# Performance work log

Measured on AMD Instinct MI355X. Metric: run time of the kernel, lower is better.

Reference implementation:

```python
import jax, jax.numpy as jnp
import numpy as np

NUM_USERS = 50000
NUM_ITEMS = 20000
NUM_NODES = NUM_USERS + NUM_ITEMS
FEAT_DIM = 768
HID = 128
NUM_LAYERS = 3
N_EDGES = 2_000_000
LN_EPS = 1e-5


def setup_inputs() -> dict:
    key = jax.random.key(0)
    ks = jax.random.split(key, 12)
    edge_index = jax.random.randint(ks[0], (2, N_EDGES), 0, NUM_NODES, dtype=jnp.int64) if jax.config.jax_enable_x64 else jax.random.randint(ks[0], (2, N_EDGES), 0, NUM_NODES, dtype=jnp.int32)
    item_features = jax.random.normal(ks[1], (NUM_ITEMS, FEAT_DIM), dtype=jnp.float32)
    embedding = jax.random.normal(ks[2], (NUM_NODES, HID), dtype=jnp.float32) * 0.1
    W1 = jax.random.normal(ks[3], (FEAT_DIM, 512), dtype=jnp.float32) * 0.02
    b1 = jnp.zeros((512,), jnp.float32)
    g1 = jnp.ones((512,), jnp.float32)
    be1 = jnp.zeros((512,), jnp.float32)
    W2 = jax.random.normal(ks[4], (512, HID), dtype=jnp.float32) * 0.02
    b2 = jnp.zeros((HID,), jnp.float32)
    g2 = jnp.ones((HID,), jnp.float32)
    be2 = jnp.zeros((HID,), jnp.float32)
    W3 = jax.random.normal(ks[5], (HID, HID), dtype=jnp.float32) * 0.02
    b3 = jnp.zeros((HID,), jnp.float32)
    meta_weight = jnp.asarray(0.01, jnp.float32)
    return {"edge_index": edge_index, "item_features": item_features, "embedding": embedding,
            "W1": W1, "b1": b1, "g1": g1, "be1": be1,
            "W2": W2, "b2": b2, "g2": g2, "be2": be2,
            "W3": W3, "b3": b3, "meta_weight": meta_weight}


def _layer_norm(x, g, b):
    mu = jnp.mean(x, axis=-1, keepdims=True)
    var = jnp.mean(jnp.square(x - mu), axis=-1, keepdims=True)
    return (x - mu) * jax.lax.rsqrt(var + LN_EPS) * g + b


def reference(edge_index, item_features, embedding, W1, b1, g1, be1, W2, b2, g2, be2, W3, b3, meta_weight):
    # item metadata MLP (eval mode: dropout is identity)
    h = jax.nn.relu(_layer_norm(item_features @ W1 + b1, g1, be1))
    h = jax.nn.relu(_layer_norm(h @ W2 + b2, g2, be2))
    h = h @ W3 + b3
    # F.normalize(p=2, dim=-1)
    item_meta = h / jnp.maximum(jnp.linalg.norm(h, axis=-1, keepdims=True), 1e-12)

    # fuse metadata into item id embeddings
    e0 = jnp.concatenate([embedding[:NUM_USERS],
                          embedding[NUM_USERS:] + meta_weight * item_meta], axis=0)

    src, dst = edge_index[0], edge_index[1]
    # symmetric GCN normalization: deg from destination counts
    deg = jax.ops.segment_sum(jnp.ones(src.shape[0], e0.dtype), dst, num_segments=NUM_NODES)
    dinv = jnp.where(deg > 0, jax.lax.rsqrt(jnp.maximum(deg, 1.0)), 0.0)
    norm = (dinv[src] * dinv[dst])[:, None]  # [E, 1]

    alpha = 1.0 / (NUM_LAYERS + 1)
    out = e0 * alpha
    x = e0
    for _ in range(NUM_LAYERS):
        x = jax.ops.segment_sum(x[src] * norm, dst, num_segments=NUM_NODES)
        out = out + x * alpha
    return out
```

## Files before the change

### kernel.cpp

```cpp
#include <hip/hip_runtime.h>
#include <hip/hip_bf16.h>

#define NUM_USERS 50000
#define NUM_ITEMS 20000
#define NUM_NODES (NUM_USERS + NUM_ITEMS)
#define FEAT_DIM 768
#define HID 128
#define H1DIM 512
#define LN_EPS 1e-5f
#define ALPHA 0.25f
#define NBKT 137

typedef __attribute__((ext_vector_type(8))) short short8;
typedef __attribute__((ext_vector_type(4))) float floatx4;

static __device__ inline unsigned short f2bf(float f) {
  unsigned int u = __float_as_uint(f);
  u += 0x7fffu + ((u >> 16) & 1u);
  return (unsigned short)(u >> 16);
}
static __device__ inline float bflo(unsigned int u) {
  return __uint_as_float(u << 16);
}
static __device__ inline float bfhi(unsigned int u) {
  return __uint_as_float(u & 0xffff0000u);
}

__global__ __launch_bounds__(256) void cast_bf16(
    const float* __restrict__ in, unsigned short* __restrict__ out) {
  size_t i = (size_t)blockIdx.x * 256 + threadIdx.x;
  float4 u = ((const float4*)in)[i * 2];
  float4 v = ((const float4*)in)[i * 2 + 1];
  union { unsigned short s[8]; uint4 q; } p;
  p.s[0] = f2bf(u.x); p.s[1] = f2bf(u.y); p.s[2] = f2bf(u.z); p.s[3] = f2bf(u.w);
  p.s[4] = f2bf(v.x); p.s[5] = f2bf(v.y); p.s[6] = f2bf(v.z); p.s[7] = f2bf(v.w);
  ((uint4*)out)[i] = p.q;
}

__global__ __launch_bounds__(256) void transpose_cast(
    const float* __restrict__ W, unsigned short* __restrict__ Wt,
    int K, int N) {
  __shared__ float tile[32][33];
  int tx = threadIdx.x, ty = threadIdx.y;
  int bx = blockIdx.x, by = blockIdx.y;
#pragma unroll
  for (int kk = 0; kk < 4; kk++)
    tile[ty + kk * 8][tx] = W[(size_t)(by * 32 + ty + kk * 8) * N + bx * 32 + tx];
  __syncthreads();
#pragma unroll
  for (int kk = 0; kk < 4; kk++)
    Wt[(size_t)(bx * 32 + ty + kk * 8) * K + by * 32 + tx] =
        f2bf(tile[tx][ty + kk * 8]);
}

__global__ __launch_bounds__(256) void gemm_mfma_bias(
    const unsigned short* __restrict__ A, const unsigned short* __restrict__ Bt,
    const float* __restrict__ bias, float* __restrict__ C,
    int M, int N, int K) {
  __shared__ __align__(16) unsigned short As[128 * 32];
  __shared__ __align__(16) unsigned short Bs[128 * 32];
  const int tid = threadIdx.x;
  const int wave = tid >> 6, lane = tid & 63;
  const int quad = lane >> 4, l16 = lane & 15;
  const int wm = wave >> 1, wn = wave & 1;
  const int bm = blockIdx.y * 128, bn = blockIdx.x * 128;

  floatx4 acc[4][4];
#pragma unroll
  for (int i = 0; i < 4; i++)
#pragma unroll
    for (int j = 0; j < 4; j++) acc[i][j] = (floatx4){0.f, 0.f, 0.f, 0.f};

  const int srow = lane >> 2;
  const int scol = (lane & 3) * 8;

  for (int k0 = 0; k0 < K; k0 += 32) {
#pragma unroll
    for (int i = 0; i < 2; i++) {
      int c = wave * 2 + i;
      int arow = bm + c * 16 + srow;
      if (arow >= M) arow = M - 1;
      const unsigned short* ga = A + (size_t)arow * K + k0 + scol;
      __builtin_amdgcn_global_load_lds(
          (const __attribute__((address_space(1))) unsigned int*)(uintptr_t)ga,
          (__attribute__((address_space(3))) unsigned int*)(uintptr_t)(As + c * 512),
          16, 0, 0);
      int brow = bn + c * 16 + srow;
      const unsigned short* gb = Bt + (size_t)brow * K + k0 + scol;
      __builtin_amdgcn_global_load_lds(
          (const __attribute__((address_space(1))) unsigned int*)(uintptr_t)gb,
          (__attribute__((address_space(3))) unsigned int*)(uintptr_t)(Bs + c * 512),
          16, 0, 0);
    }
    __syncthreads();

    short8 af[4], bf[4];
#pragma unroll
    for (int i = 0; i < 4; i++) {
      af[i] = *(const short8*)&As[(wm * 64 + i * 16 + l16) * 32 + quad * 8];
      bf[i] = *(const short8*)&Bs[(wn * 64 + i * 16 + l16) * 32 + quad * 8];
    }
#pragma unroll
    for (int i = 0; i < 4; i++)
#pragma unroll
      for (int j = 0; j < 4; j++)
        acc[i][j] = __builtin_amdgcn_mfma_f32_16x16x32_bf16(af[i], bf[j],
                                                            acc[i][j], 0, 0, 0);
    __syncthreads();
  }

#pragma unroll
  for (int i = 0; i < 4; i++) {
    int row0 = bm + wm * 64 + i * 16 + quad * 4;
#pragma unroll
    for (int j = 0; j < 4; j++) {
      int col = bn + wn * 64 + j * 16 + l16;
      float bv = bias[col];
#pragma unroll
      for (int r = 0; r < 4; r++) {
        int row = row0 + r;
        if (row < M) C[(size_t)row * N + col] = acc[i][j][r] + bv;
      }
    }
  }
}

__global__ __launch_bounds__(256) void ln_relu_w512_bf16(
    const float* __restrict__ X, const float* __restrict__ g,
    const float* __restrict__ be, unsigned short* __restrict__ O) {
  int row = blockIdx.x, t = threadIdx.x;
  const float* x = X + (size_t)row * H1DIM;
  float v0 = x[t], v1 = x[t + 256];
  float s = v0 + v1, q = v0 * v0 + v1 * v1;
#pragma unroll
  for (int off = 32; off > 0; off >>= 1) {
    s += __shfl_down(s, off);
    q += __shfl_down(q, off);
  }
  __shared__ float ss[4], qq[4];
  int lane = t & 63, wid = t >> 6;
  if (lane == 0) { ss[wid] = s; qq[wid] = q; }
  __syncthreads();
  float S = ss[0] + ss[1] + ss[2] + ss[3];
  float Q = qq[0] + qq[1] + qq[2] + qq[3];
  float mu = S * (1.f / 512.f);
  float var = Q * (1.f / 512.f) - mu * mu;
  float rs = rsqrtf(var + LN_EPS);
  float y0 = (v0 - mu) * rs * g[t] + be[t];
  float y1 = (v1 - mu) * rs * g[t + 256] + be[t + 256];
  unsigned short* o = O + (size_t)row * H1DIM;
  o[t] = f2bf(fmaxf(y0, 0.f));
  o[t + 256] = f2bf(fmaxf(y1, 0.f));
}

__global__ __launch_bounds__(256) void ln_relu_w128(
    float* __restrict__ X, const float* __restrict__ g,
    const float* __restrict__ be, int rows) {
  int gwid = (blockIdx.x * blockDim.x + threadIdx.x) >> 6;
  if (gwid >= rows) return;
  int lane = threadIdx.x & 63;
  float* x = X + (size_t)gwid * HID;
  float v0 = x[lane], v1 = x[lane + 64];
  float s = v0 + v1, q = v0 * v0 + v1 * v1;
#pragma unroll
  for (int off = 32; off > 0; off >>= 1) {
    s += __shfl_down(s, off);
    q += __shfl_down(q, off);
  }
  s = __shfl(s, 0);
  q = __shfl(q, 0);
  float mu = s * (1.f / 128.f);
  float var = q * (1.f / 128.f) - mu * mu;
  float rs = rsqrtf(var + LN_EPS);
  float y0 = (v0 - mu) * rs * g[lane] + be[lane];
  float y1 = (v1 - mu) * rs * g[lane + 64] + be[lane + 64];
  x[lane] = fmaxf(y0, 0.f);
  x[lane + 64] = fmaxf(y1, 0.f);
}

__global__ __launch_bounds__(128) void gemm3_norm4(
    const float* __restrict__ H, const float* __restrict__ W3,
    const float* __restrict__ b3, float* __restrict__ meta) {
  int r0 = blockIdx.x * 4, t = threadIdx.x;
  __shared__ float hrow[4][HID];
#pragma unroll
  for (int r = 0; r < 4; r++) hrow[r][t] = H[(size_t)(r0 + r) * HID + t];
  __syncthreads();
  float s0 = 0.f, s1 = 0.f, s2 = 0.f, s3 = 0.f;
#pragma unroll 4
  for (int k = 0; k < HID; k++) {
    float w = W3[k * HID + t];
    s0 = fmaf(hrow[0][k], w, s0);
    s1 = fmaf(hrow[1][k], w, s1);
    s2 = fmaf(hrow[2][k], w, s2);
    s3 = fmaf(hrow[3][k], w, s3);
  }
  float b = b3[t];
  s0 += b; s1 += b; s2 += b; s3 += b;
  float q0 = s0 * s0, q1 = s1 * s1, q2 = s2 * s2, q3 = s3 * s3;
#pragma unroll
  for (int off = 32; off > 0; off >>= 1) {
    q0 += __shfl_down(q0, off);
    q1 += __shfl_down(q1, off);
    q2 += __shfl_down(q2, off);
    q3 += __shfl_down(q3, off);
  }
  __shared__ float qs[4][2];
  if ((t & 63) == 0) {
    int w = t >> 6;
    qs[0][w] = q0; qs[1][w] = q1; qs[2][w] = q2; qs[3][w] = q3;
  }
  __syncthreads();
  float n0 = fmaxf(sqrtf(qs[0][0] + qs[0][1]), 1e-12f);
  float n1 = fmaxf(sqrtf(qs[1][0] + qs[1][1]), 1e-12f);
  float n2 = fmaxf(sqrtf(qs[2][0] + qs[2][1]), 1e-12f);
  float n3 = fmaxf(sqrtf(qs[3][0] + qs[3][1]), 1e-12f);
  meta[(size_t)(r0 + 0) * HID + t] = s0 / n0;
  meta[(size_t)(r0 + 1) * HID + t] = s1 / n1;
  meta[(size_t)(r0 + 2) * HID + t] = s2 / n2;
  meta[(size_t)(r0 + 3) * HID + t] = s3 / n3;
}

__global__ __launch_bounds__(256) void build_e0(
    const float* __restrict__ emb, const float* __restrict__ meta,
    const float* __restrict__ mw_p, float* __restrict__ x0,
    float* __restrict__ out) {
  size_t i = (size_t)blockIdx.x * 256 + threadIdx.x;
  float e = emb[i];
  size_t node = i >> 7;
  if (node >= NUM_USERS) e += mw_p[0] * meta[i - (size_t)NUM_USERS * HID];
  x0[i] = e;
  out[i] = ALPHA * e;
}

__global__ __launch_bounds__(256) void p1_hist(const int* __restrict__ dst,
                                               int* __restrict__ ghist,
                                               int E, int NBL) {
  __shared__ int h[NBKT];
  int t = threadIdx.x;
  if (t < NBKT) h[t] = 0;
  __syncthreads();
  int base = blockIdx.x * 8192;
  for (int i = t; i < 8192; i += 256) {
    int e = base + i;
    if (e < E) atomicAdd(&h[dst[e] >> 9], 1);
  }
  __syncthreads();
  if (t < NBKT) ghist[t * NBL + blockIdx.x] = h[t];
}

__global__ __launch_bounds__(256) void scan_a(const int* __restrict__ in,
                                              int* __restrict__ outp,
                                              int* __restrict__ bsum, int n) {
  int i = blockIdx.x * 256 + threadIdx.x;
  int v = (i < n) ? in[i] : 0;
  int lane = threadIdx.x & 63, wid = threadIdx.x >> 6;
  int s = v;
#pragma unroll
  for (int off = 1; off < 64; off <<= 1) {
    int u = __shfl_up(s, off);
    if (lane >= off) s += u;
  }
  __shared__ int wsum[4];
  if (lane == 63) wsum[wid] = s;
  __syncthreads();
  int add = 0;
  for (int w = 0; w < wid; w++) add += wsum[w];
  int incl = s + add;
  if (i < n) outp[i] = incl - v;
  if (threadIdx.x == 255) bsum[blockIdx.x] = incl;
}

__global__ __launch_bounds__(512) void scan_b(int* __restrict__ bsum, int nb) {
  int t = threadIdx.x;
  int v = (t < nb) ? bsum[t] : 0;
  int lane = t & 63, wid = t >> 6;
  int s = v;
#pragma unroll
  for (int off = 1; off < 64; off <<= 1) {
    int u = __shfl_up(s, off);
    if (lane >= off) s += u;
  }
  __shared__ int ws[8];
  if (lane == 63) ws[wid] = s;
  __syncthreads();
  int add = 0;
  for (int w = 0; w < wid; w++) add += ws[w];
  if (t < nb) bsum[t] = s + add - v;
}

__global__ __launch_bounds__(256) void scan_c(int* __restrict__ outp,
                                              const int* __restrict__ bsum,
                                              int n) {
  int i = blockIdx.x * 256 + threadIdx.x;
  if (i < n) outp[i] += bsum[blockIdx.x];
}

__global__ __launch_bounds__(256) void p1_scatter(
    const int* __restrict__ src, const int* __restrict__ dst,
    const int* __restrict__ gscan, unsigned long long* __restrict__ pairs,
    int E, int NBL) {
  __shared__ int cur[NBKT];
  int t = threadIdx.x;
  if (t < NBKT) cur[t] = gscan[t * NBL + blockIdx.x];
  __syncthreads();
  int base = blockIdx.x * 8192;
  for (int i = t; i < 8192; i += 256) {
    int e = base + i;
    if (e < E) {
      int d = dst[e];
      int pos = atomicAdd(&cur[d >> 9], 1);
      pairs[pos] = ((unsigned long long)(unsigned)d << 32) | (unsigned)src[e];
    }
  }
}

__global__ __launch_bounds__(512) void p2_build(
    const unsigned long long* __restrict__ pairs,
    const int* __restrict__ gscan, int* __restrict__ rowptr,
    int* __restrict__ csr_src, int E, int NBL) {
  __shared__ int hist[512];
  __shared__ int ws8[8];
  int b = blockIdx.x, t = threadIdx.x;
  int base = gscan[b * NBL];
  int end = (b == NBKT - 1) ? E : gscan[(b + 1) * NBL];
  hist[t] = 0;
  __syncthreads();
  for (int i = base + t; i < end; i += 512) {
    unsigned d = (unsigned)(pairs[i] >> 32);
    atomicAdd(&hist[d & 511], 1);
  }
  __syncthreads();
  int v = hist[t];
  int lane = t & 63, wid = t >> 6;
  int s = v;
#pragma unroll
  for (int off = 1; off < 64; off <<= 1) {
    int u = __shfl_up(s, off);
    if (lane >= off) s += u;
  }
  if (lane == 63) ws8[wid] = s;
  __syncthreads();
  int add = 0;
  for (int w = 0; w < wid; w++) add += ws8[w];
  int excl = s + add - v;
  int node = (b << 9) + t;
  if (node < NUM_NODES) rowptr[node] = base + excl;
  if (b == NBKT - 1 && t == 0) rowptr[NUM_NODES] = E;
  __syncthreads();
  hist[t] = base + excl;
  __syncthreads();
  for (int i = base + t; i < end; i += 512) {
    unsigned long long p = pairs[i];
    unsigned d = (unsigned)(p >> 32);
    int pos = atomicAdd(&hist[d & 511], 1);
    csr_src[pos] = (int)(unsigned)p;
  }
}

__global__ __launch_bounds__(256) void calc_dinv2(const int* __restrict__ rowptr,
                                                  float* __restrict__ dinv,
                                                  int n) {
  int i = blockIdx.x * 256 + threadIdx.x;
  if (i < n) {
    int d = rowptr[i + 1] - rowptr[i];
    dinv[i] = d > 0 ? rsqrtf((float)d) : 0.f;
  }
}

template <int XBF>
__global__ __launch_bounds__(256) void spmm_prop(
    const int* __restrict__ rowptr, const int* __restrict__ csr_src,
    const float* __restrict__ dinv, const void* __restrict__ xv,
    unsigned short* __restrict__ y, float* __restrict__ out, int write_y) {
  int wid = (blockIdx.x * 256 + threadIdx.x) >> 6;
  int lane = threadIdx.x & 63;
  int half = lane >> 5, q = lane & 31;
  int row = wid * 2 + half;
  int beg = rowptr[row], end = rowptr[row + 1];
  float wd = dinv[row];
  float a0 = 0.f, a1 = 0.f, a2 = 0.f, a3 = 0.f;
  int p = beg;
  if (XBF) {
    const unsigned short* xq = (const unsigned short*)xv + q * 4;
    for (; p + 4 <= end; p += 4) {
      int s0 = csr_src[p], s1 = csr_src[p + 1];
      int s2 = csr_src[p + 2], s3 = csr_src[p + 3];
      float c0 = dinv[s0], c1 = dinv[s1], c2 = dinv[s2], c3 = dinv[s3];
      uint2 v0 = *(const uint2*)(xq + (size_t)s0 * HID);
      uint2 v1 = *(const uint2*)(xq + (size_t)s1 * HID);
      uint2 v2 = *(const uint2*)(xq + (size_t)s2 * HID);
      uint2 v3 = *(const uint2*)(xq + (size_t)s3 * HID);
      a0 += c0 * bflo(v0.x) + c1 * bflo(v1.x) + c2 * bflo(v2.x) + c3 * bflo(v3.x);
      a1 += c0 * bfhi(v0.x) + c1 * bfhi(v1.x) + c2 * bfhi(v2.x) + c3 * bfhi(v3.x);
      a2 += c0 * bflo(v0.y) + c1 * bflo(v1.y) + c2 * bflo(v2.y) + c3 * bflo(v3.y);
      a3 += c0 * bfhi(v0.y) + c1 * bfhi(v1.y) + c2 * bfhi(v2.y) + c3 * bfhi(v3.y);
    }
    for (; p < end; p++) {
      int s0 = csr_src[p];
      float c0 = dinv[s0];
      uint2 v0 = *(const uint2*)(xq + (size_t)s0 * HID);
      a0 += c0 * bflo(v0.x); a1 += c0 * bfhi(v0.x);
      a2 += c0 * bflo(v0.y); a3 += c0 * bfhi(v0.y);
    }
  } else {
    const float* xq = (const float*)xv + q * 4;
    for (; p + 4 <= end; p += 4) {
      int s0 = csr_src[p], s1 = csr_src[p + 1];
      int s2 = csr_src[p + 2], s3 = csr_src[p + 3];
      float c0 = dinv[s0], c1 = dinv[s1], c2 = dinv[s2], c3 = dinv[s3];
      float4 v0 = *(const float4*)(xq + (size_t)s0 * HID);
      float4 v1 = *(const float4*)(xq + (size_t)s1 * HID);
      float4 v2 = *(const float4*)(xq + (size_t)s2 * HID);
      float4 v3 = *(const float4*)(xq + (size_t)s3 * HID);
      a0 += c0 * v0.x + c1 * v1.x + c2 * v2.x + c3 * v3.x;
      a1 += c0 * v0.y + c1 * v1.y + c2 * v2.y + c3 * v3.y;
      a2 += c0 * v0.z + c1 * v1.z + c2 * v2.z + c3 * v3.z;
      a3 += c0 * v0.w + c1 * v1.w + c2 * v2.w + c3 * v3.w;
    }
    for (; p < end; p++) {
      int s0 = csr_src[p];
      float c0 = dinv[s0];
      float4 v0 = *(const float4*)(xq + (size_t)s0 * HID);
      a0 += c0 * v0.x; a1 += c0 * v0.y; a2 += c0 * v0.z; a3 += c0 * v0.w;
    }
  }
  a0 *= wd; a1 *= wd; a2 *= wd; a3 *= wd;
  size_t o = (size_t)row * HID + q * 4;
  if (write_y) {
    union { unsigned short s[4]; uint2 u; } pk;
    pk.s[0] = f2bf(a0); pk.s[1] = f2bf(a1);
    pk.s[2] = f2bf(a2); pk.s[3] = f2bf(a3);
    *(uint2*)&y[o] = pk.u;
  }
  float4 po = *(const float4*)&out[o];
  po.x += ALPHA * a0; po.y += ALPHA * a1;
  po.z += ALPHA * a2; po.w += ALPHA * a3;
  *(float4*)&out[o] = po;
}

extern "C" void kernel_launch(void* const* d_in, const int* in_sizes, int n_in,
                              void* d_out, int out_size, void* d_ws,
                              size_t ws_size, hipStream_t stream) {
  const int* edge = (const int*)d_in[0];
  const float* item_feat = (const float*)d_in[1];
  const float* emb = (const float*)d_in[2];
  const float* W1 = (const float*)d_in[3];
  const float* b1 = (const float*)d_in[4];
  const float* g1 = (const float*)d_in[5];
  const float* be1 = (const float*)d_in[6];
  const float* W2 = (const float*)d_in[7];
  const float* b2 = (const float*)d_in[8];
  const float* g2 = (const float*)d_in[9];
  const float* be2 = (const float*)d_in[10];
  const float* W3 = (const float*)d_in[11];
  const float* b3 = (const float*)d_in[12];
  const float* mw = (const float*)d_in[13];
  float* out = (float*)d_out;

  const int E = in_sizes[0] / 2;
  const int* src = edge;
  const int* dst = edge + E;
  const int NBL = (E + 8191) / 8192;
  const int nScan = NBKT * NBL;
  const int NBs = (nScan + 255) / 256;

  char* ws = (char*)d_ws;
  float* h1 = (float*)(ws + 0);
  float* h2 = (float*)(ws + 40960000);
  unsigned short* h1b = (unsigned short*)(ws + 51200000);
  float* xAf = (float*)(ws + 51200000);
  unsigned short* Af = (unsigned short*)(ws + 87040000);
  unsigned short* xBb = (unsigned short*)(ws + 87040000);
  unsigned short* xCb = (unsigned short*)(ws + 104960000);
  unsigned short* W1t = (unsigned short*)(ws + 122880000);
  unsigned short* W2t = (unsigned short*)(ws + 123666432);
  float* meta = h1;

  unsigned long long* pairs = (unsigned long long*)(ws + 0);
  int* rowptr = (int*)(ws + 16000000);
  float* dinv = (float*)(ws + 16500000);
  int* ghist = (int*)(ws + 16800000);
  int* gscan = (int*)(ws + 17000000);
  int* bsum = (int*)(ws + 17200000);
  int* csr_src = (int*)(ws + 17500000);

  cast_bf16<<<(NUM_ITEMS * FEAT_DIM / 8) / 256, 256, 0, stream>>>(item_feat, Af);
  transpose_cast<<<dim3(H1DIM / 32, FEAT_DIM / 32), dim3(32, 8), 0, stream>>>(
      W1, W1t, FEAT_DIM, H1DIM);
  transpose_cast<<<dim3(HID / 32, H1DIM / 32), dim3(32, 8), 0, stream>>>(
      W2, W2t, H1DIM, HID);

  gemm_mfma_bias<<<dim3(H1DIM / 128, (NUM_ITEMS + 127) / 128), 256, 0, stream>>>(
      Af, W1t, b1, h1, NUM_ITEMS, H1DIM, FEAT_DIM);
  ln_relu_w512_bf16<<<NUM_ITEMS, 256, 0, stream>>>(h1, g1, be1, h1b);
  gemm_mfma_bias<<<dim3(HID / 128, (NUM_ITEMS + 127) / 128), 256, 0, stream>>>(
      h1b, W2t, b2, h2, NUM_ITEMS, HID, H1DIM);
  ln_relu_w128<<<(NUM_ITEMS * 64) / 256, 256, 0, stream>>>(h2, g2, be2,
                                                           NUM_ITEMS);
  gemm3_norm4<<<NUM_ITEMS / 4, 128, 0, stream>>>(h2, W3, b3, meta);

  build_e0<<<(NUM_NODES * HID) / 256, 256, 0, stream>>>(emb, meta, mw, xAf, out);

  p1_hist<<<NBL, 256, 0, stream>>>(dst, ghist, E, NBL);
  scan_a<<<NBs, 256, 0, stream>>>(ghist, gscan, bsum, nScan);
  scan_b<<<1, 512, 0, stream>>>(bsum, NBs);
  scan_c<<<NBs, 256, 0, stream>>>(gscan, bsum, nScan);
  p1_scatter<<<NBL, 256, 0, stream>>>(src, dst, gscan, pairs, E, NBL);
  p2_build<<<NBKT, 512, 0, stream>>>(pairs, gscan, rowptr, csr_src, E, NBL);
  calc_dinv2<<<(NUM_NODES + 255) / 256, 256, 0, stream>>>(rowptr, dinv,
                                                          NUM_NODES);

  const int PG = (NUM_NODES / 2 * 64) / 256;
  spmm_prop<0><<<PG, 256, 0, stream>>>(rowptr, csr_src, dinv, xAf, xBb, out, 1);
  spmm_prop<1><<<PG, 256, 0, stream>>>(rowptr, csr_src, dinv, xBb, xCb, out, 1);
  spmm_prop<1><<<PG, 256, 0, stream>>>(rowptr, csr_src, dinv, xCb, nullptr, out,
                                       0);
}
```

Baseline: 651.1 us.

## Store propagation features in chunk-major bf16 layout and split SpMM by feature chunk

The layer-0 features are now written as bf16 in a chunk-major layout (8 chunks of 16 features per node), and the SpMM kernel handles one feature chunk per block, with 8 lanes per row. Each chunk's gather footprint (about 2.2 MB) can then stay cache-resident while random source rows are read, instead of scattering across the full 128-wide rows. The cost is that each row's CSR indices and dinv values are re-read 8 times, one per chunk, and each gather is now 32 bytes. The first layer also reads bf16 instead of fp32, which lowers precision.

```diff
diff --git a/kernel.cpp b/kernel.cpp
--- a/kernel.cpp
+++ b/kernel.cpp
@@ -221,16 +221,25 @@
   meta[(size_t)(r0 + 3) * HID + t] = s3 / n3;
 }
 
-__global__ __launch_bounds__(256) void build_e0(
+__global__ __launch_bounds__(256) void build_e0_cm(
     const float* __restrict__ emb, const float* __restrict__ meta,
-    const float* __restrict__ mw_p, float* __restrict__ x0,
+    const float* __restrict__ mw_p, unsigned int* __restrict__ x0c,
     float* __restrict__ out) {
   size_t i = (size_t)blockIdx.x * 256 + threadIdx.x;
-  float e = emb[i];
-  size_t node = i >> 7;
-  if (node >= NUM_USERS) e += mw_p[0] * meta[i - (size_t)NUM_USERS * HID];
-  x0[i] = e;
-  out[i] = ALPHA * e;
+  int node = (int)(i >> 6);
+  int u6 = (int)(i & 63);
+  int chunk = u6 >> 3, fl = u6 & 7;
+  int f0 = chunk * 16 + fl * 2;
+  float2 e = *(const float2*)&emb[(size_t)node * HID + f0];
+  if (node >= NUM_USERS) {
+    float2 m = *(const float2*)&meta[(size_t)(node - NUM_USERS) * HID + f0];
+    float w = mw_p[0];
+    e.x += w * m.x;
+    e.y += w * m.y;
+  }
+  *(float2*)&out[(size_t)node * HID + f0] = make_float2(ALPHA * e.x, ALPHA * e.y);
+  unsigned pk = (unsigned)f2bf(e.x) | ((unsigned)f2bf(e.y) << 16);
+  x0c[((size_t)chunk * NUM_NODES + node) * 8 + fl] = pk;
 }
 
 __global__ __launch_bounds__(256) void p1_hist(const int* __restrict__ dst,
@@ -368,75 +377,54 @@
   }
 }
 
-template <int XBF>
-__global__ __launch_bounds__(256) void spmm_prop(
+__global__ __launch_bounds__(256) void spmm_chunk(
     const int* __restrict__ rowptr, const int* __restrict__ csr_src,
-    const float* __restrict__ dinv, const void* __restrict__ xv,
-    unsigned short* __restrict__ y, float* __restrict__ out, int write_y) {
-  int wid = (blockIdx.x * 256 + threadIdx.x) >> 6;
-  int lane = threadIdx.x & 63;
-  int half = lane >> 5, q = lane & 31;
-  int row = wid * 2 + half;
-  int beg = rowptr[row], end = rowptr[row + 1];
-  float wd = dinv[row];
-  float a0 = 0.f, a1 = 0.f, a2 = 0.f, a3 = 0.f;
+    const float* __restrict__ dinv, const unsigned int* __restrict__ xc,
+    unsigned int* __restrict__ yc, float* __restrict__ out, int write_y) {
+  int chunk = blockIdx.x & 7;
+  int rowblk = blockIdx.x >> 3;
+  int tid = threadIdx.x;
+  int wave = tid >> 6, lane = tid & 63;
+  int slot = lane >> 3, fl = lane & 7;
+  int row = rowblk * 32 + wave * 8 + slot;
+  bool act = row < NUM_NODES;
+  int rr = act ? row : NUM_NODES - 1;
+  int beg = rowptr[rr], end = rowptr[rr + 1];
+  float wd = dinv[rr];
+  const unsigned int* xq = xc + (size_t)chunk * NUM_NODES * 8 + fl;
+  float a0 = 0.f, a1 = 0.f;
   int p = beg;
-  if (XBF) {
-    const unsigned short* xq = (const unsigned short*)xv + q * 4;
-    for (; p + 4 <= end; p += 4) {
-      int s0 = csr_src[p], s1 = csr_src[p + 1];
-      int s2 = csr_src[p + 2], s3 = csr_src[p + 3];
-      float c0 = dinv[s0], c1 = dinv[s1], c2 = dinv[s2], c3 = dinv[s3];
-      uint2 v0 = *(const uint2*)(xq + (size_t)s0 * HID);
-      uint2 v1 = *(const uint2*)(xq + (size_t)s1 * HID);
-      uint2 v2 = *(const uint2*)(xq + (size_t)s2 * HID);
-      uint2 v3 = *(const uint2*)(xq + (size_t)s3 * HID);
-      a0 += c0 * bflo(v0.x) + c1 * bflo(v1.x) + c2 * bflo(v2.x) + c3 * bflo(v3.x);
-      a1 += c0 * bfhi(v0.x) + c1 * bfhi(v1.x) + c2 * bfhi(v2.x) + c3 * bfhi(v3.x);
-      a2 += c0 * bflo(v0.y) + c1 * bflo(v1.y) + c2 * bflo(v2.y) + c3 * bflo(v3.y);
-      a3 += c0 * bfhi(v0.y) + c1 * bfhi(v1.y) + c2 * bfhi(v2.y) + c3 * bfhi(v3.y);
+  for (; p + 4 <= end; p += 4) {
+    int s0 = csr_src[p], s1 = csr_src[p + 1];
+    int s2 = csr_src[p + 2], s3 = csr_src[p + 3];
+    float c0 = dinv[s0], c1 = dinv[s1], c2 = dinv[s2], c3 = dinv[s3];
+    unsigned v0 = xq[(size_t)s0 * 8];
+    unsigned v1 = xq[(size_t)s1 * 8];
+    unsigned v2 = xq[(size_t)s2 * 8];
+    unsigned v3 = xq[(size_t)s3 * 8];
+    a0 += c0 * bflo(v0) + c1 * bflo(v1) + c2 * bflo(v2) + c3 * bflo(v3);
+    a1 += c0 * bfhi(v0) + c1 * bfhi(v1) + c2 * bfhi(v2) + c3 * bfhi(v3);
+  }
+  for (; p < end; p++) {
+    int s0 = csr_src[p];
+    float c0 = dinv[s0];
+    unsigned v0 = xq[(size_t)s0 * 8];
+    a0 += c0 * bflo(v0);
+    a1 += c0 * bfhi(v0);
+  }
+  a0 *= wd;
+  a1 *= wd;
+  if (act) {
+    if (write_y) {
+      unsigned pk = (unsigned)f2bf(a0) | ((unsigned)f2bf(a1) << 16);
+      yc[((size_t)chunk * NUM_NODES + row) * 8 + fl] = pk;
     }
-    for (; p < end; p++) {
-      int s0 = csr_src[p];
-      float c0 = dinv[s0];
-      uint2 v0 = *(const uint2*)(xq + (size_t)s0 * HID);
-      a0 += c0 * bflo(v0.x); a1 += c0 * bfhi(v0.x);
-      a2 += c0 * bflo(v0.y); a3 += c0 * bfhi(v0.y);
-    }
-  } else {
-    const float* xq = (const float*)xv + q * 4;
-    for (; p + 4 <= end; p += 4) {
-      int s0 = csr_src[p], s1 = csr_src[p + 1];
-      int s2 = csr_src[p + 2], s3 = csr_src[p + 3];
-      float c0 = dinv[s0], c1 = dinv[s1], c2 = dinv[s2], c3 = dinv[s3];
-      float4 v0 = *(const float4*)(xq + (size_t)s0 * HID);
-      float4 v1 = *(const float4*)(xq + (size_t)s1 * HID);
-      float4 v2 = *(const float4*)(xq + (size_t)s2 * HID);
-      float4 v3 = *(const float4*)(xq + (size_t)s3 * HID);
-      a0 += c0 * v0.x + c1 * v1.x + c2 * v2.x + c3 * v3.x;
-      a1 += c0 * v0.y + c1 * v1.y + c2 * v2.y + c3 * v3.y;
-      a2 += c0 * v0.z + c1 * v1.z + c2 * v2.z + c3 * v3.z;
-      a3 += c0 * v0.w + c1 * v1.w + c2 * v2.w + c3 * v3.w;
-    }
-    for (; p < end; p++) {
-      int s0 = csr_src[p];
-      float c0 = dinv[s0];
-      float4 v0 = *(const float4*)(xq + (size_t)s0 * HID);
-      a0 += c0 * v0.x; a1 += c0 * v0.y; a2 += c0 * v0.z; a3 += c0 * v0.w;
-    }
-  }
-  a0 *= wd; a1 *= wd; a2 *= wd; a3 *= wd;
-  size_t o = (size_t)row * HID + q * 4;
-  if (write_y) {
-    union { unsigned short s[4]; uint2 u; } pk;
-    pk.s[0] = f2bf(a0); pk.s[1] = f2bf(a1);
-    pk.s[2] = f2bf(a2); pk.s[3] = f2bf(a3);
-    *(uint2*)&y[o] = pk.u;
-  }
-  float4 po = *(const float4*)&out[o];
-  po.x += ALPHA * a0; po.y += ALPHA * a1;
-  po.z += ALPHA * a2; po.w += ALPHA * a3;
-  *(float4*)&out[o] = po;
+    float2* op = (float2*)&out[(size_t)row * HID + chunk * 16 + fl * 2];
+    float2 po = *op;
+    po.x += ALPHA * a0;
+    po.y += ALPHA * a1;
+    *op = po;
+  }
 }
 
 extern "C" void kernel_launch(void* const* d_in, const int* in_sizes, int n_in,
@@ -469,10 +457,10 @@
   float* h1 = (float*)(ws + 0);
   float* h2 = (float*)(ws + 40960000);
   unsigned short* h1b = (unsigned short*)(ws + 51200000);
-  float* xAf = (float*)(ws + 51200000);
+  unsigned int* xA = (unsigned int*)(ws + 51200000);
   unsigned short* Af = (unsigned short*)(ws + 87040000);
-  unsigned short* xBb = (unsigned short*)(ws + 87040000);
-  unsigned short* xCb = (unsigned short*)(ws + 104960000);
+  unsigned int* xB = (unsigned int*)(ws + 87040000);
+  unsigned int* xC = (unsigned int*)(ws + 104960000);
   unsigned short* W1t = (unsigned short*)(ws + 122880000);
   unsigned short* W2t = (unsigned short*)(ws + 123666432);
   float* meta = h1;
@@ -500,7 +488,8 @@
                                                            NUM_ITEMS);
   gemm3_norm4<<<NUM_ITEMS / 4, 128, 0, stream>>>(h2, W3, b3, meta);
 
-  build_e0<<<(NUM_NODES * HID) / 256, 256, 0, stream>>>(emb, meta, mw, xAf, out);
+  build_e0_cm<<<(NUM_NODES * 64) / 256, 256, 0, stream>>>(emb, meta, mw, xA,
+                                                          out);
 
   p1_hist<<<NBL, 256, 0, stream>>>(dst, ghist, E, NBL);
   scan_a<<<NBs, 256, 0, stream>>>(ghist, gscan, bsum, nScan);
@@ -511,9 +500,8 @@
   calc_dinv2<<<(NUM_NODES + 255) / 256, 256, 0, stream>>>(rowptr, dinv,
                                                           NUM_NODES);
 
-  const int PG = (NUM_NODES / 2 * 64) / 256;
-  spmm_prop<0><<<PG, 256, 0, stream>>>(rowptr, csr_src, dinv, xAf, xBb, out, 1);
-  spmm_prop<1><<<PG, 256, 0, stream>>>(rowptr, csr_src, dinv, xBb, xCb, out, 1);
-  spmm_prop<1><<<PG, 256, 0, stream>>>(rowptr, csr_src, dinv, xCb, nullptr, out,
-                                       0);
-}
+  const int RG = ((NUM_NODES + 31) / 32) * 8;
+  spmm_chunk<<<RG, 256, 0, stream>>>(rowptr, csr_src, dinv, xA, xB, out, 1);
+  spmm_chunk<<<RG, 256, 0, stream>>>(rowptr, csr_src, dinv, xB, xC, out, 1);
+  spmm_chunk<<<RG, 256, 0, stream>>>(rowptr, csr_src, dinv, xC, nullptr, out, 0);
+}
```

After: 810.0 us. 1.24x slower.
